# Optimization experiments

Hardware: AMD Instinct MI355X
Metric: run time of the kernel (lower is better)

The kernel has to match this reference:

```python
import jax, jax.numpy as jnp
import numpy as np

CLASS_PERIOD = 360  # window width per object class


def setup_inputs() -> dict:
    key = jax.random.key(0)
    k1, k2, k3 = jax.random.split(key, 3)
    B, C, P = 16384, 12, CLASS_PERIOD
    preds = jax.random.normal(k1, (B, C * P), dtype=jnp.float32)
    labels = jax.random.uniform(k2, (B, C * P), dtype=jnp.float32)
    obj_classes = jax.random.randint(k3, (B,), 0, C, dtype=jnp.int64)
    return {"preds": preds, "labels": labels, "obj_classes": obj_classes}


def reference(preds, labels, obj_classes):
    P = CLASS_PERIOD
    # gather per-sample window of width P starting at obj_class * P
    idx = obj_classes[:, None] * P + jnp.arange(P)[None, :]  # [B, P]
    pw = jnp.take_along_axis(preds, idx, axis=1)             # [B, P]
    lw = jnp.take_along_axis(labels, idx, axis=1)            # [B, P]
    # scale by L1 norm of the window, then log-softmax over the window
    scaled = pw / jnp.sum(jnp.abs(pw), axis=1, keepdims=True)
    ls = jax.nn.log_softmax(scaled, axis=1)
    # mean=False branch: per-instance sum, accumulated (negated) over batch
    loss = -jnp.sum(lw * ls)
    return loss.reshape(1)
```

## Files before the change

### kernel.cpp

```cpp
#include <hip/hip_runtime.h>
#include <math.h>

#define CLASS_P 360
#define ROW_STRIDE 4320
#define NF4 90

__device__ __forceinline__ float wave_sum(float v) {
    #pragma unroll
    for (int o = 32; o > 0; o >>= 1) v += __shfl_xor(v, o);
    return v;
}
__device__ __forceinline__ float wave_max(float v) {
    #pragma unroll
    for (int o = 32; o > 0; o >>= 1) v = fmaxf(v, __shfl_xor(v, o));
    return v;
}

__global__ __launch_bounds__(256) void vp_loss_rows(
        const float* __restrict__ preds,
        const float* __restrict__ labels,
        const int*   __restrict__ cls,
        float* __restrict__ partial,
        int B) {
    const int row  = blockIdx.x * 4 + (threadIdx.x >> 6);
    const int lane = threadIdx.x & 63;
    if (row >= B) return;

    const size_t base = (size_t)row * ROW_STRIDE + (size_t)cls[row] * CLASS_P;
    const float4* __restrict__ p4 = (const float4*)(preds + base);
    const float4* __restrict__ l4 = (const float4*)(labels + base);

    float4 a0 = p4[lane];
    float4 b0 = l4[lane];
    const bool has2 = lane < (NF4 - 64);
    float4 a1 = make_float4(0.f, 0.f, 0.f, 0.f);
    float4 b1 = a1;
    if (has2) { a1 = p4[lane + 64]; b1 = l4[lane + 64]; }

    float sabs = fabsf(a0.x) + fabsf(a0.y) + fabsf(a0.z) + fabsf(a0.w);
    float pmax = fmaxf(fmaxf(a0.x, a0.y), fmaxf(a0.z, a0.w));
    if (has2) {
        sabs += fabsf(a1.x) + fabsf(a1.y) + fabsf(a1.z) + fabsf(a1.w);
        pmax  = fmaxf(pmax, fmaxf(fmaxf(a1.x, a1.y), fmaxf(a1.z, a1.w)));
    }
    sabs = wave_sum(sabs);
    pmax = wave_max(pmax);

    const float inv = 1.0f / sabs;
    const float m   = pmax * inv;

    float se = __expf(a0.x * inv - m) + __expf(a0.y * inv - m)
             + __expf(a0.z * inv - m) + __expf(a0.w * inv - m);
    if (has2)
        se += __expf(a1.x * inv - m) + __expf(a1.y * inv - m)
            + __expf(a1.z * inv - m) + __expf(a1.w * inv - m);
    se = wave_sum(se);
    const float lse = __logf(se) + m;

    float acc = b0.x * (lse - a0.x * inv) + b0.y * (lse - a0.y * inv)
              + b0.z * (lse - a0.z * inv) + b0.w * (lse - a0.w * inv);
    if (has2)
        acc += b1.x * (lse - a1.x * inv) + b1.y * (lse - a1.y * inv)
             + b1.z * (lse - a1.z * inv) + b1.w * (lse - a1.w * inv);
    acc = wave_sum(acc);

    if (lane == 0) partial[row] = acc;
}

__global__ __launch_bounds__(512) void vp_loss_reduce(
        const float* __restrict__ partial, float* __restrict__ out, int n) {
    __shared__ float sm[8];
    float acc = 0.f;
    for (int i = threadIdx.x; i < n; i += 512) acc += partial[i];
    acc = wave_sum(acc);
    const int wid = threadIdx.x >> 6, lane = threadIdx.x & 63;
    if (lane == 0) sm[wid] = acc;
    __syncthreads();
    if (wid == 0) {
        float v = (lane < 8) ? sm[lane] : 0.f;
        v = wave_sum(v);
        if (lane == 0) out[0] = v;
    }
}

extern "C" void kernel_launch(void* const* d_in, const int* in_sizes, int n_in,
                              void* d_out, int out_size, void* d_ws, size_t ws_size,
                              hipStream_t stream) {
    const float* preds  = (const float*)d_in[0];
    const float* labels = (const float*)d_in[1];
    const int*   cls    = (const int*)d_in[2];
    float* out = (float*)d_out;
    float* ws  = (float*)d_ws;

    const int B = in_sizes[2];
    const int blocks = (B + 3) / 4;

    vp_loss_rows<<<blocks, 256, 0, stream>>>(preds, labels, cls, ws, B);
    vp_loss_reduce<<<1, 512, 0, stream>>>(ws, out, B);
}
```

Measured before the change: 24.03 us.

## Process four rows per wave with batched loads and per-block partial sums

Each wave now handles four rows and issues all of their loads up front, giving more memory-level parallelism per wave. Each block then reduces its four wave results in shared memory, so the partial buffer is much smaller and the final single-block reduction has less work. The cost is more registers per thread, which may lower occupancy, and a grid of a quarter as many blocks.

```diff
diff --git a/kernel.cpp b/kernel.cpp
--- a/kernel.cpp
+++ b/kernel.cpp
@@ -4,6 +4,7 @@
 #define CLASS_P 360
 #define ROW_STRIDE 4320
 #define NF4 90
+#define RPW 4
 
 __device__ __forceinline__ float wave_sum(float v) {
     #pragma unroll
@@ -16,71 +17,83 @@
     return v;
 }
 
-__global__ __launch_bounds__(256) void vp_loss_rows(
+__global__ __launch_bounds__(256) void vp_rows(
         const float* __restrict__ preds,
         const float* __restrict__ labels,
         const int*   __restrict__ cls,
         float* __restrict__ partial,
         int B) {
-    const int row  = blockIdx.x * 4 + (threadIdx.x >> 6);
+    const int wid  = threadIdx.x >> 6;
     const int lane = threadIdx.x & 63;
-    if (row >= B) return;
+    const int wave = blockIdx.x * 4 + wid;
+    const int r0   = wave * RPW;
+    const bool has2 = lane < (NF4 - 64);
 
-    const size_t base = (size_t)row * ROW_STRIDE + (size_t)cls[row] * CLASS_P;
-    const float4* __restrict__ p4 = (const float4*)(preds + base);
-    const float4* __restrict__ l4 = (const float4*)(labels + base);
+    float4 a0[RPW], b0[RPW], a1[RPW], b1[RPW];
+    float  wgt[RPW];
 
-    float4 a0 = p4[lane];
-    float4 b0 = l4[lane];
-    const bool has2 = lane < (NF4 - 64);
-    float4 a1 = make_float4(0.f, 0.f, 0.f, 0.f);
-    float4 b1 = a1;
-    if (has2) { a1 = p4[lane + 64]; b1 = l4[lane + 64]; }
+    #pragma unroll
+    for (int k = 0; k < RPW; k++) {
+        const int r  = r0 + k;
+        const int rr = (r < B) ? r : 0;
+        wgt[k] = (r < B) ? 1.0f : 0.0f;
+        const size_t base = (size_t)rr * ROW_STRIDE + (size_t)cls[rr] * CLASS_P;
+        const float4* __restrict__ p4 = (const float4*)(preds + base);
+        const float4* __restrict__ l4 = (const float4*)(labels + base);
+        a0[k] = p4[lane];
+        b0[k] = l4[lane];
+        a1[k] = make_float4(0.f, 0.f, 0.f, 0.f);
+        b1[k] = a1[k];
+        if (has2) { a1[k] = p4[lane + 64]; b1[k] = l4[lane + 64]; }
+    }
 
-    float sabs = fabsf(a0.x) + fabsf(a0.y) + fabsf(a0.z) + fabsf(a0.w);
-    float pmax = fmaxf(fmaxf(a0.x, a0.y), fmaxf(a0.z, a0.w));
-    if (has2) {
-        sabs += fabsf(a1.x) + fabsf(a1.y) + fabsf(a1.z) + fabsf(a1.w);
-        pmax  = fmaxf(pmax, fmaxf(fmaxf(a1.x, a1.y), fmaxf(a1.z, a1.w)));
+    float acc = 0.f;
+    #pragma unroll
+    for (int k = 0; k < RPW; k++) {
+        float sabs = fabsf(a0[k].x) + fabsf(a0[k].y) + fabsf(a0[k].z) + fabsf(a0[k].w)
+                   + fabsf(a1[k].x) + fabsf(a1[k].y) + fabsf(a1[k].z) + fabsf(a1[k].w);
+        float pmax = fmaxf(fmaxf(a0[k].x, a0[k].y), fmaxf(a0[k].z, a0[k].w));
+        if (has2)
+            pmax = fmaxf(pmax, fmaxf(fmaxf(a1[k].x, a1[k].y), fmaxf(a1[k].z, a1[k].w)));
+        sabs = wave_sum(sabs);
+        pmax = wave_max(pmax);
+
+        const float inv = 1.0f / sabs;
+        const float m   = pmax * inv;
+
+        float se = __expf(a0[k].x * inv - m) + __expf(a0[k].y * inv - m)
+                 + __expf(a0[k].z * inv - m) + __expf(a0[k].w * inv - m);
+        if (has2)
+            se += __expf(a1[k].x * inv - m) + __expf(a1[k].y * inv - m)
+                + __expf(a1[k].z * inv - m) + __expf(a1[k].w * inv - m);
+        se = wave_sum(se);
+        const float lse = __logf(se) + m;
+
+        float t = b0[k].x * (lse - a0[k].x * inv) + b0[k].y * (lse - a0[k].y * inv)
+                + b0[k].z * (lse - a0[k].z * inv) + b0[k].w * (lse - a0[k].w * inv);
+        if (has2)
+            t += b1[k].x * (lse - a1[k].x * inv) + b1[k].y * (lse - a1[k].y * inv)
+               + b1[k].z * (lse - a1[k].z * inv) + b1[k].w * (lse - a1[k].w * inv);
+        acc += wgt[k] * t;
     }
-    sabs = wave_sum(sabs);
-    pmax = wave_max(pmax);
-
-    const float inv = 1.0f / sabs;
-    const float m   = pmax * inv;
-
-    float se = __expf(a0.x * inv - m) + __expf(a0.y * inv - m)
-             + __expf(a0.z * inv - m) + __expf(a0.w * inv - m);
-    if (has2)
-        se += __expf(a1.x * inv - m) + __expf(a1.y * inv - m)
-            + __expf(a1.z * inv - m) + __expf(a1.w * inv - m);
-    se = wave_sum(se);
-    const float lse = __logf(se) + m;
-
-    float acc = b0.x * (lse - a0.x * inv) + b0.y * (lse - a0.y * inv)
-              + b0.z * (lse - a0.z * inv) + b0.w * (lse - a0.w * inv);
-    if (has2)
-        acc += b1.x * (lse - a1.x * inv) + b1.y * (lse - a1.y * inv)
-             + b1.z * (lse - a1.z * inv) + b1.w * (lse - a1.w * inv);
     acc = wave_sum(acc);
 
-    if (lane == 0) partial[row] = acc;
+    __shared__ float sm[4];
+    if (lane == 0) sm[wid] = acc;
+    __syncthreads();
+    if (threadIdx.x == 0) partial[blockIdx.x] = sm[0] + sm[1] + sm[2] + sm[3];
 }
 
-__global__ __launch_bounds__(512) void vp_loss_reduce(
+__global__ __launch_bounds__(256) void vp_reduce(
         const float* __restrict__ partial, float* __restrict__ out, int n) {
-    __shared__ float sm[8];
+    __shared__ float sm[4];
     float acc = 0.f;
-    for (int i = threadIdx.x; i < n; i += 512) acc += partial[i];
+    for (int i = threadIdx.x; i < n; i += 256) acc += partial[i];
     acc = wave_sum(acc);
     const int wid = threadIdx.x >> 6, lane = threadIdx.x & 63;
     if (lane == 0) sm[wid] = acc;
     __syncthreads();
-    if (wid == 0) {
-        float v = (lane < 8) ? sm[lane] : 0.f;
-        v = wave_sum(v);
-        if (lane == 0) out[0] = v;
-    }
+    if (threadIdx.x == 0) out[0] = sm[0] + sm[1] + sm[2] + sm[3];
 }
 
 extern "C" void kernel_launch(void* const* d_in, const int* in_sizes, int n_in,
@@ -93,8 +106,9 @@
     float* ws  = (float*)d_ws;
 
     const int B = in_sizes[2];
-    const int blocks = (B + 3) / 4;
+    const int rows_per_block = 4 * RPW;
+    const int blocks = (B + rows_per_block - 1) / rows_per_block;
 
-    vp_loss_rows<<<blocks, 256, 0, stream>>>(preds, labels, cls, ws, B);
-    vp_loss_reduce<<<1, 512, 0, stream>>>(ws, out, B);
+    vp_rows<<<blocks, 256, 0, stream>>>(preds, labels, cls, ws, B);
+    vp_reduce<<<1, 256, 0, stream>>>(ws, out, blocks);
 }
```

After: 19.66 us. 18.2% less time.
